# Kernel optimization log

Measured on AMD Instinct MI355X. Metric: run time of the kernel, lower is better.

Reference implementation:

```python
import jax, jax.numpy as jnp
import numpy as np

K = 16  # hard-coded neighborhood size
EPS = 1e-5


def knn_idx(coor_k, coor_q, k):
    # coor_*: (B, 3, N). Returns idx (B, Nq, k) of k nearest points in coor_k for each query.
    inner = jnp.einsum('bcn,bcm->bnm', coor_q, coor_k)
    sq_q = jnp.sum(coor_q ** 2, axis=1)  # (B, Nq)
    sq_k = jnp.sum(coor_k ** 2, axis=1)  # (B, Nk)
    dist = sq_q[:, :, None] + sq_k[:, None, :] - 2.0 * inner  # (B, Nq, Nk)
    return jax.lax.top_k(-dist, k)[1]


def fps(coor, num_group):
    # furthest point sampling, matching pointnet2 (start at index 0, squared dists).
    B, _, N = coor.shape
    xyz = jnp.transpose(coor, (0, 2, 1))  # (B, N, 3)

    def step(carry, _):
        dist, last = carry
        centroid = jnp.take_along_axis(xyz, last[:, None, None], axis=1)  # (B,1,3)
        d = jnp.sum((xyz - centroid) ** 2, axis=-1)  # (B, N)
        dist = jnp.minimum(dist, d)
        nxt = jnp.argmax(dist, axis=1).astype(jnp.int32)
        return (dist, nxt), last

    init = (jnp.full((B, N), 1e10, dtype=coor.dtype), jnp.zeros((B,), jnp.int32))
    _, idxs = jax.lax.scan(step, init, None, length=num_group)
    return jnp.transpose(idxs, (1, 0))  # (B, num_group)


def gather_points(x, idx):
    # x: (B, C, N), idx: (B, S) -> (B, C, S)
    return jnp.take_along_axis(x, idx[:, None, :], axis=2)


def get_graph_feature(coor_q, x_q, coor_k, x_k):
    # coor: (B,3,N), x: (B,C,N) -> (B, 2C, Nq, K)
    B, C, Nq = x_q.shape
    idx = jax.lax.stop_gradient(knn_idx(coor_k, coor_q, K))  # (B, Nq, K)
    idx_flat = jnp.broadcast_to(idx.reshape(B, 1, Nq * K), (B, C, Nq * K))
    nbr = jnp.take_along_axis(x_k, idx_flat, axis=2).reshape(B, C, Nq, K)
    xq = x_q[..., None]  # (B, C, Nq, 1)
    return jnp.concatenate([nbr - xq, jnp.broadcast_to(xq, nbr.shape)], axis=1)


def group_norm(x, gamma, beta, groups):
    # x: (B, C, N, K); normalize over (C//G, N, K) per sample per group.
    B, C = x.shape[0], x.shape[1]
    xr = x.reshape(B, groups, C // groups, *x.shape[2:])
    red = tuple(range(2, xr.ndim))
    mean = jnp.mean(xr, axis=red, keepdims=True)
    var = jnp.mean((xr - mean) ** 2, axis=red, keepdims=True)
    xn = ((xr - mean) * jax.lax.rsqrt(var + EPS)).reshape(x.shape)
    shp = (1, C) + (1,) * (x.ndim - 2)
    return xn * gamma.reshape(shp) + beta.reshape(shp)


def lrelu(x):
    return jnp.where(x >= 0, x, 0.2 * x)


def edge_layer(f, w, g, b):
    # 1x1 conv (no bias) + GroupNorm(4) + LeakyReLU(0.2)
    f = jnp.einsum('oc,bcnk->bonk', w, f)
    return lrelu(group_norm(f, g, b, 4))


def setup_inputs() -> dict:
    key = jax.random.key(0)
    ks = jax.random.split(key, 16)
    B, N = 32, 2048
    p = {}
    p['x'] = jax.random.normal(ks[0], (B, 3, N), dtype=jnp.float32)
    p['w_in'] = jax.random.normal(ks[1], (8, 3), dtype=jnp.float32) * 0.3
    p['b_in'] = jax.random.normal(ks[2], (8,), dtype=jnp.float32) * 0.1
    dims = [(32, 16), (64, 64), (64, 128), (128, 128)]
    for i, (o, c) in enumerate(dims, start=1):
        kw, kg, kb = jax.random.split(ks[2 + i], 3)
        p[f'w{i}'] = jax.random.normal(kw, (o, c), dtype=jnp.float32) * (1.0 / np.sqrt(c))
        p[f'g{i}'] = 1.0 + 0.1 * jax.random.normal(kg, (o,), dtype=jnp.float32)
        p[f'b{i}'] = 0.1 * jax.random.normal(kb, (o,), dtype=jnp.float32)
    return p


def reference(x, w_in, b_in, w1, g1, b1, w2, g2, b2, w3, g3, b3, w4, g4, b4):
    coor = x
    f = jnp.einsum('oc,bcn->bon', w_in, x) + b_in[None, :, None]  # (B,8,N)

    f = get_graph_feature(coor, f, coor, f)          # (B,16,N,K)
    f = jnp.max(edge_layer(f, w1, g1, b1), axis=-1)  # (B,32,N)

    idx = jax.lax.stop_gradient(fps(coor, 512))
    coor_q, f_q = gather_points(coor, idx), gather_points(f, idx)
    f = get_graph_feature(coor_q, f_q, coor, f)      # (B,64,512,K)
    f = jnp.max(edge_layer(f, w2, g2, b2), axis=-1)  # (B,64,512)
    coor = coor_q

    f = get_graph_feature(coor, f, coor, f)          # (B,128,512,K)
    f = jnp.max(edge_layer(f, w3, g3, b3), axis=-1)  # (B,64,512)

    idx = jax.lax.stop_gradient(fps(coor, 128))
    coor_q, f_q = gather_points(coor, idx), gather_points(f, idx)
    f = get_graph_feature(coor_q, f_q, coor, f)      # (B,128,128,K)
    f = jnp.max(edge_layer(f, w4, g4, b4), axis=-1)  # (B,128,128)
    coor = coor_q
    return coor, f
```

## Files before the change

kernel.cpp:

```cpp
#include <hip/hip_runtime.h>
#include <hip/hip_bf16.h>

#define DEV __device__ __forceinline__
typedef unsigned long long u64;

DEV float bf2f(unsigned short u){ return __uint_as_float(((unsigned)u)<<16); }
DEV unsigned short f2bf(float f){
  unsigned u = __float_as_uint(f);
  u += 0x7fffu + ((u>>16)&1u);
  return (unsigned short)(u>>16);
}

template<int CTRL>
DEV u64 dpp_umax(u64 k){
  int lo = (int)(unsigned)k;
  int hi = (int)(unsigned)(k>>32);
  int plo = __builtin_amdgcn_update_dpp(lo, lo, CTRL, 0xF, 0xF, false);
  int phi = __builtin_amdgcn_update_dpp(hi, hi, CTRL, 0xF, 0xF, false);
  u64 p = ((u64)(unsigned)phi << 32) | (unsigned)plo;
  return (p > k) ? p : k;
}

DEV void ce64(u64 &a, u64 &b){
  u64 lo = (a<b)?a:b;
  u64 hi = (a<b)?b:a;
  a = lo; b = hi;
}
DEV void sort8(u64* x){
  #pragma unroll
  for (int k=2;k<=8;k<<=1){
    #pragma unroll
    for (int j=k>>1;j>0;j>>=1){
      #pragma unroll
      for (int i=0;i<8;++i){
        int l = i^j;
        if (l>i){
          if ((i&k)==0) ce64(x[i],x[l]);
          else          ce64(x[l],x[i]);
        }
      }
    }
  }
}
DEV void bm16(u64* A){
  #pragma unroll
  for (int gap=8;gap>0;gap>>=1){
    #pragma unroll
    for (int i=0;i<16;++i){
      if ((i&gap)==0) ce64(A[i], A[i|gap]);
    }
  }
}
DEV unsigned f2sort(float d){
  unsigned ub = __float_as_uint(d);
  unsigned s  = (unsigned)((int)ub >> 31);
  return ub ^ (s | 0x80000000u);
}

struct PConv {
  const void* s[14];
  float*      d[14];
  int         sz[14];
};

__global__ __launch_bounds__(256) void prep_kernel(
    const void* __restrict__ xraw, int* __restrict__ flagw,
    const void* __restrict__ w_in_raw, const void* __restrict__ b_in_raw,
    PConv p,
    float* __restrict__ xyz0, float* __restrict__ f0, float* __restrict__ stats){
  __shared__ int cnt;
  int t = threadIdx.x;
  if (t==0) cnt = 0;
  __syncthreads();
  {
    const unsigned short* xs = (const unsigned short*)xraw;
    int local = 0;
    for (int i=t; i<4096; i+=256){
      int e = (xs[i]>>7)&0xFF;
      if (e >= 0xC0) local++;
    }
    atomicAdd(&cnt, local);
  }
  __syncthreads();
  bool isf = (cnt > 64);
  int bx = blockIdx.x;
  if (bx==0 && t==0) *flagw = isf ? 1 : 0;
  if (bx < 117){
    int i = bx*256 + t;
    int seg = 0, off = i;
    #pragma unroll
    for (seg=0; seg<14; ++seg){
      if (off < p.sz[seg]) break;
      off -= p.sz[seg];
    }
    if (seg >= 14) return;
    float v = isf ? ((const float*)p.s[seg])[off]
                  : bf2f(((const unsigned short*)p.s[seg])[off]);
    p.d[seg][off] = v;
    return;
  }
  int i = (bx-117)*256 + t;
  if (i < 8192) stats[i] = 0.f;
  int b = i >> 11, n = i & 2047;
  size_t base = (size_t)b*3*2048 + n;
  float X, Y, Z;
  if (isf){
    const float* xf = (const float*)xraw;
    X = xf[base]; Y = xf[base+2048]; Z = xf[base+4096];
  } else {
    const unsigned short* xu = (const unsigned short*)xraw;
    X = bf2f(xu[base]); Y = bf2f(xu[base+2048]); Z = bf2f(xu[base+4096]);
  }
  float* o3 = xyz0 + (size_t)i*3;
  o3[0]=X; o3[1]=Y; o3[2]=Z;
  const float* wf = (const float*)w_in_raw;
  const float* bf = (const float*)b_in_raw;
  const unsigned short* wu = (const unsigned short*)w_in_raw;
  const unsigned short* bu = (const unsigned short*)b_in_raw;
  float* fo = f0 + (size_t)i*8;
  #pragma unroll
  for (int o=0;o<8;++o){
    float w0 = isf ? wf[o*3+0] : bf2f(wu[o*3+0]);
    float w1 = isf ? wf[o*3+1] : bf2f(wu[o*3+1]);
    float w2 = isf ? wf[o*3+2] : bf2f(wu[o*3+2]);
    float bb = isf ? bf[o]     : bf2f(bu[o]);
    fo[o] = w0*X + w1*Y + w2*Z + bb;
  }
}

template<int NK, int QB>
DEV void knn_body(float* smem, const float* __restrict__ qxyz,
                  const float* __restrict__ kxyz, int Nq,
                  int* __restrict__ oidx, int bx, int b){
  float4* kd = (float4*)smem;
  u64* lbuf  = (u64*)smem;
  int t = threadIdx.x;
  for (int i=t; i<NK; i+=256){
    const float* p = kxyz + ((size_t)b*NK + i)*3;
    float X=p[0], Y=p[1], Z=p[2];
    float sk = __fadd_rn(__fadd_rn(__fmul_rn(X,X),__fmul_rn(Y,Y)),__fmul_rn(Z,Z));
    kd[i] = make_float4(X,Y,Z,sk);
  }
  __syncthreads();
  int ql = t>>2, h = t&3;
  int q0 = bx*QB;
  const float* qp = qxyz + ((size_t)b*Nq + q0 + ql)*3;
  float QX=qp[0], QY=qp[1], QZ=qp[2];
  float sq = __fadd_rn(__fadd_rn(__fmul_rn(QX,QX),__fmul_rn(QY,QY)),__fmul_rn(QZ,QZ));
  u64 A[16];
  #pragma unroll
  for (int j=0;j<16;++j) A[j] = ~0ULL;
  #pragma unroll 1
  for (int i=0; i<NK/4; i+=8){
    u64 k8[8];
    #pragma unroll
    for (int u=0;u<8;++u){
      int cidx = 4*(i+u)+h;
      float4 c = kd[cidx];
      float dot = __fadd_rn(__fadd_rn(__fmul_rn(QX,c.x),__fmul_rn(QY,c.y)),__fmul_rn(QZ,c.z));
      float d = __fsub_rn(__fadd_rn(sq, c.w), __fmul_rn(2.0f,dot));
      k8[u] = ((u64)f2sort(d)<<32) | (unsigned)cidx;
    }
    sort8(k8);
    #pragma unroll
    for (int s=0;s<8;++s){
      u64 bb = k8[7-s];
      u64 a  = A[8+s];
      A[8+s] = (bb < a) ? bb : a;
    }
    bm16(A);
  }
  __syncthreads();
  u64* Lq = lbuf + ((size_t)ql*65 + (size_t)h*16);
  #pragma unroll
  for (int j=0;j<16;++j) Lq[j] = A[j];
  __syncthreads();
  if (t < QB){
    const u64* db = lbuf + (size_t)t*65;
    int p0=0,p1=0,p2=0,p3=0;
    u64 e0=db[0], e1=db[16], e2=db[32], e3=db[48];
    int* op = oidx + ((size_t)b*Nq + q0 + t)*16;
    #pragma unroll 1
    for (int j=0;j<16;++j){
      u64 bd = e0; int bh = 0;
      if (e1 < bd){ bd=e1; bh=1; }
      if (e2 < bd){ bd=e2; bh=2; }
      if (e3 < bd){ bd=e3; bh=3; }
      op[j] = (int)(unsigned)bd;
      if      (bh==0){ p0++; e0 = (p0<16)? db[p0]    : ~0ULL; }
      else if (bh==1){ p1++; e1 = (p1<16)? db[16+p1] : ~0ULL; }
      else if (bh==2){ p2++; e2 = (p2<16)? db[32+p2] : ~0ULL; }
      else           { p3++; e3 = (p3<16)? db[48+p3] : ~0ULL; }
    }
  }
  __syncthreads();
}

template<int NP,int G>
DEV void fps_body(float* smem, const float* __restrict__ xyz,
                  int* __restrict__ oidx, float* __restrict__ oxyz, int b){
  constexpr int PPT = NP/256;
  __builtin_amdgcn_s_setprio(3);
  float4* xl4 = (float4*)smem;
  u64* candK = (u64*)(smem + NP*4);
  float4* candX = (float4*)(smem + NP*4 + 16);
  int* selidx = (int*)(smem + NP*4 + 48);
  int t = threadIdx.x, w = t>>6;
  float px[PPT], py[PPT], pz[PPT], dist[PPT];
  #pragma unroll
  for (int j=0;j<PPT;++j){
    int gi = t + j*256;
    const float* p = xyz + ((size_t)b*NP + gi)*3;
    float X=p[0], Y=p[1], Z=p[2];
    px[j]=X; py[j]=Y; pz[j]=Z; dist[j]=1e10f;
    xl4[gi] = make_float4(X,Y,Z,0.f);
  }
  if (t==0) selidx[0] = 0;
  __syncthreads();
  float4 c0 = xl4[0];
  float cx=c0.x, cy=c0.y, cz=c0.z;
  int Bi = 0;
  for (int g=1; g<G; ++g){
    float bv=-1.f; int bi=0; float bxc=0.f, byc=0.f, bzc=0.f;
    #pragma unroll
    for (int j=0;j<PPT;++j){
      float dx=__fsub_rn(px[j],cx), dy=__fsub_rn(py[j],cy), dz=__fsub_rn(pz[j],cz);
      float d = __fadd_rn(__fadd_rn(__fmul_rn(dx,dx),__fmul_rn(dy,dy)),__fmul_rn(dz,dz));
      float nd = fminf(dist[j], d);
      dist[j] = nd;
      bool cc = (nd > bv);
      bv = cc ? nd : bv;
      bi = cc ? (t + j*256) : bi;
      bxc = cc ? px[j] : bxc; byc = cc ? py[j] : byc; bzc = cc ? pz[j] : bzc;
    }
    u64 klocal = ((u64)__float_as_uint(bv) << 32) | (unsigned)(0xFFFFFFFFu - bi);
    u64 k = klocal;
    k = dpp_umax<0x111>(k);
    k = dpp_umax<0x112>(k);
    k = dpp_umax<0x114>(k);
    k = dpp_umax<0x118>(k);
    k = dpp_umax<0x142>(k);
    k = dpp_umax<0x143>(k);
    unsigned klo = (unsigned)__builtin_amdgcn_readlane((int)(unsigned)k, 63);
    unsigned khi = (unsigned)__builtin_amdgcn_readlane((int)(unsigned)(k>>32), 63);
    u64 wkey = ((u64)khi<<32) | klo;
    int par = g & 1;
    if (klocal == wkey){
      candK[par*4 + w] = wkey;
      candX[par*4 + w] = make_float4(bxc, byc, bzc, 0.f);
    }
    __syncthreads();
    u64 kk = candK[par*4+0]; float4 xx = candX[par*4+0];
    u64 k1 = candK[par*4+1]; float4 x1 = candX[par*4+1];
    if (k1 > kk){ kk=k1; xx=x1; }
    u64 k2 = candK[par*4+2]; float4 x2 = candX[par*4+2];
    if (k2 > kk){ kk=k2; xx=x2; }
    u64 k3 = candK[par*4+3]; float4 x3 = candX[par*4+3];
    if (k3 > kk){ kk=k3; xx=x3; }
    Bi = (int)(0xFFFFFFFFu - (unsigned)kk);
    cx = xx.x; cy = xx.y; cz = xx.z;
    if (t==0) selidx[g] = Bi;
  }
  __syncthreads();
  for (int i=t; i<G; i+=256){
    int s = selidx[i];
    float4 c = xl4[s];
    oidx[(size_t)b*G + i] = s;
    float* op = oxyz + ((size_t)b*G + i)*3;
    op[0]=c.x; op[1]=c.y; op[2]=c.z;
  }
}

template<int CF,int COUT,int QB>
DEV void edge_body(float* smem, const float* __restrict__ fk,
                   const int* __restrict__ sel, const int* __restrict__ knn,
                   const float* __restrict__ w, float* __restrict__ mm,
                   float* __restrict__ stats, int Nq, int Nk, int bx, int b){
  constexpr int CIN = 2*CF;
  constexpr int GPQ = COUT/2;
  constexpr int WS  = COUT+1;
  constexpr int ESTR= CF*16+8;
  constexpr int WTB = ((CF*WS+3)&~3);
  static_assert(QB*GPQ == 256, "block mapping");
  float* wtb = smem;
  float* e   = smem + WTB;
  float* fqs = e + QB*ESTR;
  float* sS  = fqs + QB*CF;
  int t = threadIdx.x;
  int q0 = bx*QB;

  if (t<8) sS[t]=0.f;
  for (int i=t; i<QB*CF; i+=256){
    int ql = i/CF, c = i&(CF-1);
    int qi = sel ? sel[b*Nq + q0 + ql] : (q0 + ql);
    fqs[i] = fk[((size_t)b*Nk + qi)*CF + c];
  }
  for (int i=t; i<CF*COUT; i+=256){
    int o = i/CF, c = i&(CF-1);
    wtb[c*WS+o] = w[o*CIN + c];
  }
  if (t < QB*16){
    int ql = t>>4, k = t&15;
    int nid = knn[((size_t)b*Nq + q0 + ql)*16 + k];
    const float4* row = (const float4*)(fk + ((size_t)b*Nk + nid)*CF);
    float* ep = e + ql*ESTR + k;
    #pragma unroll
    for (int c4=0; c4<CF/4; ++c4){
      float4 v = row[c4];
      ep[(c4*4+0)*16]=v.x; ep[(c4*4+1)*16]=v.y; ep[(c4*4+2)*16]=v.z; ep[(c4*4+3)*16]=v.w;
    }
  }
  __syncthreads();

  int ql = t/GPQ, o = t%GPQ;
  const float* eb = e + ql*ESTR;
  const float* fqb = fqs + ql*CF;
  float y0[16], y1[16];
  #pragma unroll
  for (int k=0;k<16;++k){ y0[k]=0.f; y1[k]=0.f; }
  float zA0=0.f, zA1=0.f;
  for (int c=0;c<CF;++c){
    float w0 = wtb[c*WS+o];
    float w1 = wtb[c*WS+o+GPQ];
    float fqc = fqb[c];
    zA0 = fmaf(w0,fqc,zA0); zA1 = fmaf(w1,fqc,zA1);
    const float4* ev4 = (const float4*)(eb + c*16);
    #pragma unroll
    for (int k4=0;k4<4;++k4){
      float4 ev = ev4[k4];
      y0[k4*4+0]=fmaf(w0,ev.x,y0[k4*4+0]); y0[k4*4+1]=fmaf(w0,ev.y,y0[k4*4+1]);
      y0[k4*4+2]=fmaf(w0,ev.z,y0[k4*4+2]); y0[k4*4+3]=fmaf(w0,ev.w,y0[k4*4+3]);
      y1[k4*4+0]=fmaf(w1,ev.x,y1[k4*4+0]); y1[k4*4+1]=fmaf(w1,ev.y,y1[k4*4+1]);
      y1[k4*4+2]=fmaf(w1,ev.z,y1[k4*4+2]); y1[k4*4+3]=fmaf(w1,ev.w,y1[k4*4+3]);
    }
  }
  __syncthreads();
  for (int i=t; i<CF*COUT; i+=256){
    int oo = i/CF, c = i&(CF-1);
    wtb[c*WS+oo] = w[oo*CIN + CF + c];
  }
  __syncthreads();
  float zB0=0.f, zB1=0.f;
  for (int c=0;c<CF;++c){
    float fqc = fqb[c];
    zB0 = fmaf(wtb[c*WS+o],fqc,zB0);
    zB1 = fmaf(wtb[c*WS+o+GPQ],fqc,zB1);
  }
  float z0 = zB0 - zA0, z1 = zB1 - zA1;

  float mx0=-3.4e38f, mn0=3.4e38f, s0=0.f, q0s=0.f;
  float mx1=-3.4e38f, mn1=3.4e38f, s1=0.f, q1s=0.f;
  #pragma unroll
  for (int k=0;k<16;++k){
    float v0 = y0[k]+z0, v1 = y1[k]+z1;
    mx0=fmaxf(mx0,v0); mn0=fminf(mn0,v0); s0+=v0; q0s=fmaf(v0,v0,q0s);
    mx1=fmaxf(mx1,v1); mn1=fminf(mn1,v1); s1+=v1; q1s=fmaf(v1,v1,q1s);
  }
  int g0 = o/(COUT/4);
  atomicAdd(&sS[g0],   s0); atomicAdd(&sS[4+g0],   q0s);
  atomicAdd(&sS[g0+2], s1); atomicAdd(&sS[6+g0],   q1s);
  size_t mi0 = ((size_t)b*Nq + q0 + ql)*COUT + o;
  ((float2*)mm)[mi0]       = make_float2(mx0,mn0);
  ((float2*)mm)[mi0+GPQ]   = make_float2(mx1,mn1);
  __syncthreads();
  if (t<8){
    int g = t>>1, which = t&1;
    float val = which ? sS[4+g] : sS[g];
    atomicAdd(&stats[(((size_t)b*4+g)*8 + (bx&7))*2 + which], val);
  }
}

DEV void coor_body(const float* __restrict__ xyz2, void* __restrict__ outbase,
                   const int* __restrict__ flag, int bx){
  int i = bx*256 + threadIdx.x;
  if (i >= 12288) return;
  int m = i & 127;
  int c = (i>>7) % 3;
  int b = i / 384;
  float v = xyz2[((size_t)b*128+m)*3 + c];
  if (*flag) ((float*)outbase)[i] = v;
  else       ((unsigned short*)outbase)[i] = f2bf(v);
}

__global__ __launch_bounds__(256,4) void fused1_kernel(
    const float* __restrict__ xyz0, int* __restrict__ knnb1,
    int* __restrict__ idx1, float* __restrict__ xyz1){
  __shared__ __align__(16) float smem[8752];
  int bx = blockIdx.x;
  if (bx < 32){
    fps_body<2048,512>(smem, xyz0, idx1, xyz1, bx);
  } else {
    int rid = bx - 32;
    knn_body<2048,64>(smem, xyz0, xyz0, 2048, knnb1, rid & 31, rid >> 5);
  }
}

__global__ __launch_bounds__(256,4) void fused2_kernel(
    const float* __restrict__ xyz0, const float* __restrict__ xyz1,
    const int* __restrict__ knnb1,
    int* __restrict__ knnb2, int* __restrict__ knnb3,
    int* __restrict__ idx2, float* __restrict__ xyz2,
    const float* __restrict__ f0, const float* __restrict__ cw1,
    float* __restrict__ mmb, float* __restrict__ stats1){
  __shared__ __align__(16) float smem[8320];
  int bx = blockIdx.x;
  if (bx < 32){
    fps_body<512,128>(smem, xyz1, idx2, xyz2, bx);
  } else if (bx < 288){
    int rid = bx - 32;
    knn_body<2048,64>(smem, xyz1, xyz0, 512, knnb2, rid & 7, rid >> 3);
  } else if (bx < 544){
    int rid = bx - 288;
    knn_body<512,64>(smem, xyz1, xyz1, 512, knnb3, rid & 7, rid >> 3);
  } else {
    int rid = bx - 544;
    edge_body<8,32,16>(smem, f0, nullptr, knnb1, cw1, mmb, stats1,
                       2048, 2048, rid & 127, rid >> 7);
  }
}

__global__ __launch_bounds__(256,4) void fused3_kernel(
    const float* __restrict__ xyz1, const float* __restrict__ xyz2,
    int* __restrict__ knnb4,
    const float* __restrict__ f1, const int* __restrict__ idx1,
    const int* __restrict__ knnb2, const float* __restrict__ cw2,
    float* __restrict__ mmb, float* __restrict__ stats2,
    void* __restrict__ outbase, const int* __restrict__ flag){
  __shared__ __align__(16) float smem[8320];
  int bx = blockIdx.x;
  if (bx < 64){
    knn_body<512,64>(smem, xyz2, xyz1, 128, knnb4, bx & 1, bx >> 1);
  } else if (bx < 2112){
    int rid = bx - 64;
    edge_body<32,64,8>(smem, f1, idx1, knnb2, cw2, mmb, stats2,
                       512, 2048, rid & 63, rid >> 6);
  } else {
    coor_body(xyz2, outbase, flag, bx - 2112);
  }
}

template<int CF,int COUT,int QB>
__global__ __launch_bounds__(256) void edge_kernel(
    const float* __restrict__ fk, const int* __restrict__ sel,
    const int* __restrict__ knn, const float* __restrict__ w,
    float* __restrict__ mm, float* __restrict__ stats, int Nq, int Nk){
  constexpr int WS  = COUT+1;
  constexpr int ESTR= CF*16+8;
  constexpr int WTB = ((CF*WS+3)&~3);
  constexpr int SM  = WTB + QB*ESTR + QB*CF + 8;
  __shared__ __align__(16) float smem[SM];
  edge_body<CF,COUT,QB>(smem, fk, sel, knn, w, mm, stats, Nq, Nk,
                        blockIdx.x, blockIdx.y);
}

__global__ __launch_bounds__(256) void fin_kernel(
    const float* __restrict__ mm, const float* __restrict__ stats,
    const float* __restrict__ gam, const float* __restrict__ bet,
    float* __restrict__ fo, void* __restrict__ outbase, const int* __restrict__ flag,
    int outoff, int Nq, int COUT, float invcnt, int total){
  for (int i = blockIdx.x*256 + threadIdx.x; i<total; i += gridDim.x*256){
    int o = i % COUT;
    int r = i / COUT;
    int q = r % Nq;
    int b = r / Nq;
    int g = o / (COUT>>2);
    const float* sp = stats + ((size_t)(b*4+g))*16;
    float s=0.f, s2=0.f;
    #pragma unroll
    for (int nb=0;nb<8;++nb){ s += sp[nb*2]; s2 += sp[nb*2+1]; }
    float mean = s*invcnt;
    float var  = fmaxf(s2*invcnt - mean*mean, 0.f);
    float inv  = 1.0f / sqrtf(var + 1e-5f);
    float a  = gam[o] * inv;
    float bb = bet[o] - a*mean;
    const float* mp = mm + (size_t)i*2;
    float xv = (a>=0.f) ? mp[0] : mp[1];
    float v = fmaf(a, xv, bb);
    v = (v>=0.f) ? v : 0.2f*v;
    if (fo) fo[i]=v;
    if (outbase){
      int idx = outoff + ((b*COUT + o)*Nq + q);
      if (*flag) ((float*)outbase)[idx] = v;
      else       ((unsigned short*)outbase)[idx] = f2bf(v);
    }
  }
}

extern "C" void kernel_launch(void* const* d_in, const int* in_sizes, int n_in,
                              void* d_out, int out_size, void* d_ws, size_t ws_size,
                              hipStream_t stream){
  float* W    = (float*)d_ws;
  float* xyz0 = W;
  float* f0   = W + 196608;
  float* f1   = W + 720896;
  float* xyz1 = W + 2818048;
  float* f2   = W + 2867200;
  float* f3   = W + 3915776;
  float* xyz2 = W + 4964352;
  float* stats= W + 4976640;
  int*   flag = (int*)(W + 4984832);
  float* PRM  = W + 4984848;
  int*  idx1  = (int*)(W + 5014640);
  int*  idx2  = (int*)(W + 5031024);
  float* SCR  = W + 5035120;
  int*   knnb = (int*)SCR;
  int*   knnb4= (int*)SCR;
  int*   knnb2= (int*)f3;
  int*   knnb3= (int*)f3 + 262144;
  float* mmb  = SCR + 1048576;

  float* cw_in = PRM;
  float* cb_in = PRM+24;
  float* cw1 = PRM+32;   float* cg1 = PRM+544;   float* cbb1 = PRM+576;
  float* cw2 = PRM+608;  float* cg2 = PRM+4704;  float* cbb2 = PRM+4768;
  float* cw3 = PRM+4832; float* cg3 = PRM+13024; float* cbb3 = PRM+13088;
  float* cw4 = PRM+13152;float* cg4 = PRM+29536; float* cbb4 = PRM+29664;

  PConv pc;
  const int psz[14] = {24,8,512,32,32,4096,64,64,8192,64,64,16384,128,128};
  float* pdst[14] = {cw_in,cb_in,cw1,cg1,cbb1,cw2,cg2,cbb2,cw3,cg3,cbb3,cw4,cg4,cbb4};
  for (int j=0;j<14;++j){ pc.s[j]=d_in[j+1]; pc.d[j]=pdst[j]; pc.sz[j]=psz[j]; }

  prep_kernel<<<373,256,0,stream>>>(d_in[0], flag, d_in[1], d_in[2], pc,
                                    xyz0, f0, stats);

  fused1_kernel<<<1056,256,0,stream>>>(xyz0, knnb, idx1, xyz1);

  fused2_kernel<<<4640,256,0,stream>>>(xyz0, xyz1, knnb, knnb2, knnb3,
                                       idx2, xyz2, f0, cw1, mmb, stats+0);

  fin_kernel<<<1024,256,0,stream>>>(mmb, stats+0, cg1, cbb1, f1, nullptr, flag, 0, 2048, 32, 1.f/262144.f, 2097152);

  fused3_kernel<<<2160,256,0,stream>>>(xyz1, xyz2, knnb4,
                                       f1, idx1, knnb2, cw2, mmb, stats+2048,
                                       d_out, flag);
  fin_kernel<<<1024,256,0,stream>>>(mmb, stats+2048, cg2, cbb2, f2, nullptr, flag, 0, 512, 64, 1.f/131072.f, 1048576);

  edge_kernel<64,64,8><<<dim3(64,32),256,0,stream>>>(f2, nullptr, knnb3, cw3, mmb, stats+4096, 512, 512);
  fin_kernel<<<1024,256,0,stream>>>(mmb, stats+4096, cg3, cbb3, f3, nullptr, flag, 0, 512, 64, 1.f/131072.f, 1048576);

  edge_kernel<64,128,4><<<dim3(32,32),256,0,stream>>>(f3, idx2, knnb4, cw4, mmb, stats+6144, 128, 512);
  fin_kernel<<<1024,256,0,stream>>>(mmb, stats+6144, cg4, cbb4, nullptr, d_out, flag, 12288, 128, 128, 1.f/65536.f, 524288);
}
```

Measured before the change: 620.6 us.

## Replace per-iteration FPS barrier with generation-tagged LDS spin-wait reduction

Packs the iteration number, max distance and index into one 64-bit key, so each wave publishes its winner to a double-buffered LDS slot and spin-waits on the other waves' slots instead of using a block barrier. The winning centroid coordinates are then read from the shared point array by index, which drops the coordinate select and exchange. This is meant to cut barrier latency in the serial FPS loop. In exchange it adds spin-polling with s_sleep and depends on volatile LDS visibility and the limited bit widths of the key.

```diff
diff --git a/kernel.cpp b/kernel.cpp
--- a/kernel.cpp
+++ b/kernel.cpp
@@ -203,8 +203,7 @@
   __builtin_amdgcn_s_setprio(3);
   float4* xl4 = (float4*)smem;
   u64* candK = (u64*)(smem + NP*4);
-  float4* candX = (float4*)(smem + NP*4 + 16);
-  int* selidx = (int*)(smem + NP*4 + 48);
+  int* selidx = (int*)(smem + NP*4 + 16);
   int t = threadIdx.x, w = t>>6;
   float px[PPT], py[PPT], pz[PPT], dist[PPT];
   #pragma unroll
@@ -215,13 +214,14 @@
     px[j]=X; py[j]=Y; pz[j]=Z; dist[j]=1e10f;
     xl4[gi] = make_float4(X,Y,Z,0.f);
   }
+  if (t < 8) candK[t] = 0;
   if (t==0) selidx[0] = 0;
   __syncthreads();
   float4 c0 = xl4[0];
   float cx=c0.x, cy=c0.y, cz=c0.z;
   int Bi = 0;
   for (int g=1; g<G; ++g){
-    float bv=-1.f; int bi=0; float bxc=0.f, byc=0.f, bzc=0.f;
+    float bv=-1.f; int bi=0;
     #pragma unroll
     for (int j=0;j<PPT;++j){
       float dx=__fsub_rn(px[j],cx), dy=__fsub_rn(py[j],cy), dz=__fsub_rn(pz[j],cz);
@@ -231,10 +231,10 @@
       bool cc = (nd > bv);
       bv = cc ? nd : bv;
       bi = cc ? (t + j*256) : bi;
-      bxc = cc ? px[j] : bxc; byc = cc ? py[j] : byc; bzc = cc ? pz[j] : bzc;
-    }
-    u64 klocal = ((u64)__float_as_uint(bv) << 32) | (unsigned)(0xFFFFFFFFu - bi);
-    u64 k = klocal;
+    }
+    u64 k = ((u64)(unsigned)g << 54)
+          | ((u64)__float_as_uint(bv) << 22)
+          | (unsigned)(0x3FFFFFu - bi);
     k = dpp_umax<0x111>(k);
     k = dpp_umax<0x112>(k);
     k = dpp_umax<0x114>(k);
@@ -245,20 +245,22 @@
     unsigned khi = (unsigned)__builtin_amdgcn_readlane((int)(unsigned)(k>>32), 63);
     u64 wkey = ((u64)khi<<32) | klo;
     int par = g & 1;
-    if (klocal == wkey){
-      candK[par*4 + w] = wkey;
-      candX[par*4 + w] = make_float4(bxc, byc, bzc, 0.f);
-    }
-    __syncthreads();
-    u64 kk = candK[par*4+0]; float4 xx = candX[par*4+0];
-    u64 k1 = candK[par*4+1]; float4 x1 = candX[par*4+1];
-    if (k1 > kk){ kk=k1; xx=x1; }
-    u64 k2 = candK[par*4+2]; float4 x2 = candX[par*4+2];
-    if (k2 > kk){ kk=k2; xx=x2; }
-    u64 k3 = candK[par*4+3]; float4 x3 = candX[par*4+3];
-    if (k3 > kk){ kk=k3; xx=x3; }
-    Bi = (int)(0xFFFFFFFFu - (unsigned)kk);
-    cx = xx.x; cy = xx.y; cz = xx.z;
+    volatile u64* slots = candK + par*4;
+    if ((t&63)==0) slots[w] = wkey;
+    u64 kk = wkey;
+    #pragma unroll
+    for (int ow=0; ow<4; ++ow){
+      if (ow == w) continue;
+      u64 kv = slots[ow];
+      while ((unsigned)(kv>>54) != (unsigned)g){
+        __builtin_amdgcn_s_sleep(1);
+        kv = slots[ow];
+      }
+      kk = (kv > kk) ? kv : kk;
+    }
+    Bi = (int)(0x3FFFFFu - (unsigned)(kk & 0x3FFFFFu));
+    float4 c = xl4[Bi];
+    cx = c.x; cy = c.y; cz = c.z;
     if (t==0) selidx[g] = Bi;
   }
   __syncthreads();
```

After: 669.6 us. +7.9%, slower.
